# Optimization experiments

Measured on AMD Instinct MI355X. Metric: run time of the kernel, lower is better.

The kernel has to match this reference:

```python
import jax, jax.numpy as jnp
import numpy as np
import math

B, C, H, W = 16, 64, 128, 128
EPS = 1e-5


def _ln(x, g, b):
    m = jnp.mean(x, axis=-1, keepdims=True)
    v = jnp.var(x, axis=-1, keepdims=True)
    return (x - m) * jax.lax.rsqrt(v + EPS) * g + b


def setup_inputs() -> dict:
    key = jax.random.key(0)
    ks = jax.random.split(key, 8)
    s = 1.0 / math.sqrt(C)
    return {
        "x_l": jax.random.normal(ks[0], (B, C, H, W), dtype=jnp.float32),
        "x_h": jax.random.normal(ks[1], (B, C, H, W), dtype=jnp.float32),
        "ln1_g": jnp.ones((C,), jnp.float32),
        "ln1_b": jnp.zeros((C,), jnp.float32),
        "ln2_g": jnp.ones((C,), jnp.float32),
        "ln2_b": jnp.zeros((C,), jnp.float32),
        "Wq": jax.random.normal(ks[2], (C, C), dtype=jnp.float32) * s,
        "Wk": jax.random.normal(ks[3], (C, C), dtype=jnp.float32) * s,
        "Wv1": jax.random.normal(ks[4], (C, C), dtype=jnp.float32) * s,
        "Wv2": jax.random.normal(ks[5], (C, C), dtype=jnp.float32) * s,
    }


def reference(x_l, x_h, ln1_g, ln1_b, ln2_g, ln2_b, Wq, Wk, Wv1, Wv2):
    # [B,C,H,W] -> [B,H,W,C]
    xl = jnp.transpose(x_l, (0, 2, 3, 1))
    xh = jnp.transpose(x_h, (0, 2, 3, 1))
    # torch Linear: x @ W.T (no bias)
    xl_v = xl @ Wv1.T
    xh_v = xh @ Wv2.T
    q = _ln(xl, ln1_g, ln1_b) @ Wq.T
    k = _ln(xh, ln2_g, ln2_b) @ Wk.T
    # shared score matrix over the W axis: [B,H,W,W]
    attn = jnp.einsum('bhwc,bhvc->bhwv', q, k) * (1.0 / math.sqrt(C))
    attn_h = jax.nn.softmax(attn, axis=-1)                                  # row softmax
    attn_l = jax.nn.softmax(jnp.swapaxes(attn, 2, 3), axis=-1)              # column softmax
    xl_o = jnp.einsum('bhwv,bhvc->bhwc', attn_l, xl_v)
    xh_o = jnp.einsum('bhwv,bhvc->bhwc', attn_h, xh_v)
    xh_out = xh + xl_o
    xl_out = xl + xh_o
    # back to [B,C,H,W]
    return (jnp.transpose(xl_out, (0, 3, 1, 2)), jnp.transpose(xh_out, (0, 3, 1, 2)))
```

## Files before the change

kernel.cpp:

```cpp
#include <hip/hip_runtime.h>
#include <cstdint>


typedef __attribute__((ext_vector_type(8))) short bf16x8;
typedef __attribute__((ext_vector_type(4))) float f32x4;
typedef __attribute__((ext_vector_type(4))) unsigned u32x4;
typedef __attribute__((ext_vector_type(4))) unsigned short u16x4;

#define W2 136
#define QP 72
#define EP 132
#define OP 68

__device__ __forceinline__ unsigned rne_hi(float x) {
  unsigned u = __float_as_uint(x);
  return (u + 0x7FFFu + ((u >> 16) & 1u)) >> 16;
}
__device__ __forceinline__ void split2(float x, unsigned short& h, unsigned short& l) {
  unsigned hb = rne_hi(x);
  float rf = x - __uint_as_float(hb << 16);
  h = (unsigned short)hb;
  l = (unsigned short)(__float_as_uint(rf) >> 16);
}
__device__ __forceinline__ unsigned split_pack(float x) {
  unsigned short h, l; split2(x, h, l);
  return ((unsigned)h << 16) | (unsigned)l;
}
__device__ __forceinline__ float comb(unsigned h, unsigned l) {
  return __uint_as_float(h << 16) + __uint_as_float(l << 16);
}
__device__ __forceinline__ float unpack_f(unsigned p) {
  return __uint_as_float(p & 0xFFFF0000u) + __uint_as_float(p << 16);
}
__device__ __forceinline__ f32x4 mm3(bf16x8 ah, bf16x8 al, bf16x8 bh, bf16x8 bl, f32x4 c) {
  c = __builtin_amdgcn_mfma_f32_16x16x32_bf16(al, bh, c, 0, 0, 0);
  c = __builtin_amdgcn_mfma_f32_16x16x32_bf16(ah, bl, c, 0, 0, 0);
  c = __builtin_amdgcn_mfma_f32_16x16x32_bf16(ah, bh, c, 0, 0, 0);
  return c;
}

__global__ void scam_prepack(const float* __restrict__ ln1g, const float* __restrict__ ln1b,
                             const float* __restrict__ ln2g, const float* __restrict__ ln2b,
                             const float* __restrict__ Wq, const float* __restrict__ Wk,
                             const float* __restrict__ Wv1, const float* __restrict__ Wv2,
                             unsigned short* __restrict__ WP, float* __restrict__ vecs) {
  int t = blockIdx.x * 256 + threadIdx.x;
  int mat = t >> 12, rem = t & 4095, co = rem >> 6, c = rem & 63;
  const float* Ws = (mat == 0) ? Wq : (mat == 1) ? Wk : (mat == 2) ? Wv1 : Wv2;
  float g = 1.0f;
  if (mat == 0) g = ln1g[c];
  else if (mat == 1) g = ln2g[c];
  float val = Ws[co * 64 + c] * g;
  unsigned short h, l; split2(val, h, l);
  int nt = co >> 4, l15 = co & 15, ks = c >> 5, lg = (c >> 3) & 3, j = c & 7;
  int lanei = lg * 16 + l15;
  int ntk = nt * 2 + ks;
  WP[((mat * 2 + 0) * 8 + ntk) * 512 + lanei * 8 + j] = h;
  WP[((mat * 2 + 1) * 8 + ntk) * 512 + lanei * 8 + j] = l;
  if (blockIdx.x == 0 && threadIdx.x < 256) {
    int which = threadIdx.x >> 6, o = threadIdx.x & 63;
    const float* Wm = (which < 2) ? Wq : Wk;
    const float* gv = (which == 0) ? ln1g : (which == 1) ? ln1b : (which == 2) ? ln2g : ln2b;
    float ssum = 0.f;
    for (int cc = 0; cc < 64; ++cc) ssum += gv[cc] * Wm[o * 64 + cc];
    vecs[which * 64 + o] = ssum;
  }
}

struct SMem {
  unsigned short Xhi[2][64][W2];
  unsigned short Xlo[2][64][W2];
  union {
    unsigned short QK[4][128][QP];
    unsigned Epk[128][EP];
    unsigned Opk[2][128][OP];
  } rb;
  float meanv[2][128];
  float rstdv[2][128];
  float zr[128];
  float zc[128];
};

__launch_bounds__(1024, 1)
__global__ void scam_main(const float* __restrict__ xl_g, const float* __restrict__ xh_g,
                          const unsigned short* __restrict__ WP, const float* __restrict__ vecs,
                          float* __restrict__ out) {
  __shared__ __align__(16) SMem sm;
  const int tid = threadIdx.x;
  const int lane = tid & 63;
  const int wid = tid >> 6;
  const int stripe = wid >> 1;
  const int chalf = wid & 1;
  const int l15 = lane & 15;
  const int lg = lane >> 4;
  const int s = blockIdx.x;
  const size_t xoff = (size_t)(s >> 7) * 1048576u + (size_t)(s & 127) * 128u;

  {
    int c0 = tid >> 5, q4 = tid & 31;
#pragma unroll
    for (int mat = 0; mat < 2; ++mat) {
      const float* xg = mat ? xh_g : xl_g;
#pragma unroll
      for (int half = 0; half < 2; ++half) {
        int c = c0 + half * 32;
        f32x4 v = *(const f32x4*)(xg + xoff + (size_t)c * 16384u + q4 * 4);
        u16x4 h4, l4;
#pragma unroll
        for (int j = 0; j < 4; ++j) { unsigned short hh, ll; split2(v[j], hh, ll); h4[j] = hh; l4[j] = ll; }
        *(u16x4*)&sm.Xhi[mat][c][q4 * 4] = h4;
        *(u16x4*)&sm.Xlo[mat][c][q4 * 4] = l4;
      }
    }
  }
  __syncthreads();

  {
    int row = tid >> 2, qu = tid & 3;
    int mat = row >> 7, w = row & 127;
    float s1 = 0.f, s2 = 0.f;
#pragma unroll
    for (int i = 0; i < 16; ++i) {
      int c = qu * 16 + i;
      float x = comb(sm.Xhi[mat][c][w], sm.Xlo[mat][c][w]);
      s1 += x; s2 += x * x;
    }
    s1 += __shfl_xor(s1, 1); s2 += __shfl_xor(s2, 1);
    s1 += __shfl_xor(s1, 2); s2 += __shfl_xor(s2, 2);
    if (qu == 0) {
      float mn = s1 * (1.f / 64.f);
      float var = fmaxf(s2 * (1.f / 64.f) - mn * mn, 0.f);
      sm.meanv[mat][w] = mn;
      sm.rstdv[mat][w] = rsqrtf(var + 1e-5f);
    }
  }
  __syncthreads();

  {
    const int w = stripe * 16 + l15;
#pragma unroll
    for (int mat = 0; mat < 2; ++mat) {
      bf16x8 Ah[2], Al[2];
#pragma unroll
      for (int ks = 0; ks < 2; ++ks)
#pragma unroll
        for (int j = 0; j < 8; ++j) {
          int c = ks * 32 + lg * 8 + j;
          Ah[ks][j] = (short)sm.Xhi[mat][c][w];
          Al[ks][j] = (short)sm.Xlo[mat][c][w];
        }
      f32x4 acc[2];
#pragma unroll
      for (int nt = 0; nt < 2; ++nt)
#pragma unroll
        for (int r = 0; r < 4; ++r) acc[nt][r] = 0.f;
#pragma unroll
      for (int nt = 0; nt < 2; ++nt) {
        int ntg = chalf * 2 + nt;
#pragma unroll
        for (int ks = 0; ks < 2; ++ks) {
          const unsigned short* wp = WP + ((mat * 2 + 0) * 8 + (ntg * 2 + ks)) * 512 + lane * 8;
          bf16x8 Bh = *(const bf16x8*)wp;
          bf16x8 Bl = *(const bf16x8*)(wp + 4096);
          acc[nt] = mm3(Ah[ks], Al[ks], Bh, Bl, acc[nt]);
        }
      }
#pragma unroll
      for (int nt = 0; nt < 2; ++nt) {
        int co = (chalf * 2 + nt) * 16 + l15;
        float sv = vecs[mat * 128 + co];
        float bv = vecs[mat * 128 + 64 + co];
#pragma unroll
        for (int r = 0; r < 4; ++r) {
          int wr = stripe * 16 + lg * 4 + r;
          float qv = sm.rstdv[mat][wr] * (acc[nt][r] - sm.meanv[mat][wr] * sv) + bv;
          unsigned short hh, ll; split2(qv, hh, ll);
          sm.rb.QK[mat * 2 + 0][wr][co] = hh;
          sm.rb.QK[mat * 2 + 1][wr][co] = ll;
        }
      }
    }
  }
  __syncthreads();

  {
    const int w = stripe * 16 + l15;
    bf16x8 Ah[2], Al[2];
#pragma unroll
    for (int ks = 0; ks < 2; ++ks) {
      Ah[ks] = *(const bf16x8*)&sm.rb.QK[0][w][ks * 32 + lg * 8];
      Al[ks] = *(const bf16x8*)&sm.rb.QK[1][w][ks * 32 + lg * 8];
    }
    f32x4 acc[4];
#pragma unroll
    for (int nt = 0; nt < 4; ++nt)
#pragma unroll
      for (int r = 0; r < 4; ++r) acc[nt][r] = 0.f;
#pragma unroll
    for (int nt = 0; nt < 4; ++nt) {
      int kw = (chalf * 4 + nt) * 16 + l15;
#pragma unroll
      for (int ks = 0; ks < 2; ++ks) {
        bf16x8 Bh = *(const bf16x8*)&sm.rb.QK[2][kw][ks * 32 + lg * 8];
        bf16x8 Bl = *(const bf16x8*)&sm.rb.QK[3][kw][ks * 32 + lg * 8];
        acc[nt] = mm3(Ah[ks], Al[ks], Bh, Bl, acc[nt]);
      }
    }
    __syncthreads();
#pragma unroll
    for (int nt = 0; nt < 4; ++nt) {
      int col = (chalf * 4 + nt) * 16 + l15;
#pragma unroll
      for (int r = 0; r < 4; ++r) {
        int row = stripe * 16 + lg * 4 + r;
        float e = __builtin_amdgcn_exp2f(acc[nt][r] * 0.18033688011112042f);
        sm.rb.Epk[row][col] = split_pack(e);
      }
    }
  }
  __syncthreads();

  {
    int qu = tid & 3;
    float sum = 0.f;
    if (tid < 512) {
      int row = tid >> 2;
#pragma unroll
      for (int i = 0; i < 8; ++i) {
        u32x4 p = *(const u32x4*)&sm.rb.Epk[row][qu * 32 + i * 4];
#pragma unroll
        for (int j = 0; j < 4; ++j) sum += unpack_f(p[j]);
      }
      sum += __shfl_xor(sum, 1);
      sum += __shfl_xor(sum, 2);
      if (qu == 0) sm.zr[row] = 1.0f / sum;
    } else {
      int col = (tid >> 2) & 127;
#pragma unroll 8
      for (int i = 0; i < 32; ++i) sum += unpack_f(sm.rb.Epk[qu * 32 + i][col]);
      sum += __shfl_xor(sum, 1);
      sum += __shfl_xor(sum, 2);
      if (qu == 0) sm.zc[col] = 1.0f / sum;
    }
  }
  __syncthreads();

  {
    f32x4 acc0[2], acc1[2];
#pragma unroll
    for (int nt = 0; nt < 2; ++nt)
#pragma unroll
      for (int r = 0; r < 4; ++r) { acc0[nt][r] = 0.f; acc1[nt][r] = 0.f; }
#pragma unroll
    for (int kt = 0; kt < 4; ++kt) {
      {
        int row = stripe * 16 + l15;
        u32x4 p0 = *(const u32x4*)&sm.rb.Epk[row][kt * 32 + lg * 8];
        u32x4 p1 = *(const u32x4*)&sm.rb.Epk[row][kt * 32 + lg * 8 + 4];
        bf16x8 Ah, Al;
#pragma unroll
        for (int j = 0; j < 4; ++j) {
          Ah[j] = (short)(p0[j] >> 16);     Al[j] = (short)(p0[j] & 0xFFFFu);
          Ah[j + 4] = (short)(p1[j] >> 16); Al[j + 4] = (short)(p1[j] & 0xFFFFu);
        }
#pragma unroll
        for (int nt = 0; nt < 2; ++nt) {
          int c = (chalf * 2 + nt) * 16 + l15;
          bf16x8 Bh = *(const bf16x8*)&sm.Xhi[1][c][kt * 32 + lg * 8];
          bf16x8 Bl = *(const bf16x8*)&sm.Xlo[1][c][kt * 32 + lg * 8];
          acc0[nt] = mm3(Ah, Al, Bh, Bl, acc0[nt]);
        }
      }
      {
        bf16x8 Gh, Gl;
#pragma unroll
        for (int j = 0; j < 8; ++j) {
          unsigned p = sm.rb.Epk[kt * 32 + lg * 8 + j][stripe * 16 + l15];
          Gh[j] = (short)(p >> 16); Gl[j] = (short)(p & 0xFFFFu);
        }
#pragma unroll
        for (int nt = 0; nt < 2; ++nt) {
          int c = (chalf * 2 + nt) * 16 + l15;
          bf16x8 Bh = *(const bf16x8*)&sm.Xhi[0][c][kt * 32 + lg * 8];
          bf16x8 Bl = *(const bf16x8*)&sm.Xlo[0][c][kt * 32 + lg * 8];
          acc1[nt] = mm3(Gh, Gl, Bh, Bl, acc1[nt]);
        }
      }
    }
    __syncthreads();
#pragma unroll
    for (int nt = 0; nt < 2; ++nt) {
      int col = (chalf * 2 + nt) * 16 + l15;
#pragma unroll
      for (int r = 0; r < 4; ++r) {
        int row = stripe * 16 + lg * 4 + r;
        sm.rb.Opk[0][row][col] = split_pack(acc0[nt][r] * sm.zr[row]);
        sm.rb.Opk[1][row][col] = split_pack(acc1[nt][r] * sm.zc[row]);
      }
    }
  }
  __syncthreads();

#pragma unroll
  for (int oi = 0; oi < 2; ++oi) {
    const int wm = oi ? 2 : 3;
    const int w = stripe * 16 + l15;
    bf16x8 Ah[2], Al[2];
#pragma unroll
    for (int ks = 0; ks < 2; ++ks) {
      u32x4 p0 = *(const u32x4*)&sm.rb.Opk[oi][w][ks * 32 + lg * 8];
      u32x4 p1 = *(const u32x4*)&sm.rb.Opk[oi][w][ks * 32 + lg * 8 + 4];
#pragma unroll
      for (int j = 0; j < 4; ++j) {
        Ah[ks][j] = (short)(p0[j] >> 16);     Al[ks][j] = (short)(p0[j] & 0xFFFFu);
        Ah[ks][j + 4] = (short)(p1[j] >> 16); Al[ks][j + 4] = (short)(p1[j] & 0xFFFFu);
      }
    }
    f32x4 acc[2];
#pragma unroll
    for (int nt = 0; nt < 2; ++nt)
#pragma unroll
      for (int r = 0; r < 4; ++r) acc[nt][r] = 0.f;
#pragma unroll
    for (int nt = 0; nt < 2; ++nt) {
      int ntg = chalf * 2 + nt;
#pragma unroll
      for (int ks = 0; ks < 2; ++ks) {
        const unsigned short* wp = WP + ((wm * 2 + 0) * 8 + (ntg * 2 + ks)) * 512 + lane * 8;
        bf16x8 Bh = *(const bf16x8*)wp;
        bf16x8 Bl = *(const bf16x8*)(wp + 4096);
        acc[nt] = mm3(Ah[ks], Al[ks], Bh, Bl, acc[nt]);
      }
    }
    float* og = out + (size_t)oi * 16777216u + xoff;
    const int w0 = stripe * 16 + lg * 4;
#pragma unroll
    for (int nt = 0; nt < 2; ++nt) {
      int c = (chalf * 2 + nt) * 16 + l15;
      u16x4 hv = *(const u16x4*)&sm.Xhi[oi][c][w0];
      u16x4 lv = *(const u16x4*)&sm.Xlo[oi][c][w0];
      f32x4 o;
#pragma unroll
      for (int r = 0; r < 4; ++r) o[r] = acc[nt][r] + comb(hv[r], lv[r]);
      *(f32x4*)(og + (size_t)c * 16384u + w0) = o;
    }
  }
}

extern "C" void kernel_launch(void* const* d_in, const int* in_sizes, int n_in,
                              void* d_out, int out_size, void* d_ws, size_t ws_size,
                              hipStream_t stream) {
  (void)in_sizes; (void)n_in; (void)out_size; (void)ws_size;
  unsigned short* WP = (unsigned short*)d_ws;
  float* vecs = (float*)((char*)d_ws + 65536);
  scam_prepack<<<64, 256, 0, stream>>>(
      (const float*)d_in[2], (const float*)d_in[3],
      (const float*)d_in[4], (const float*)d_in[5],
      (const float*)d_in[6], (const float*)d_in[7],
      (const float*)d_in[8], (const float*)d_in[9], WP, vecs);
  scam_main<<<2048, 1024, 0, stream>>>(
      (const float*)d_in[0], (const float*)d_in[1], WP, vecs, (float*)d_out);
}
```

Baseline: 366.9 us.

## Fold Wq and Wk into one bilinear form and fuse the softmax sums

Precomputes M = Wq^T Wk (with the LN gains, LN biases and softmax scale folded in), so the scores come from LN(xl)·M applied straight against the raw xh columns. This drops one of the two 64x64 projections per block, and the xh layer norm is applied afterwards as per-column mean and rstd corrections. The row and column softmax sums are now reduced from registers during the exp stage, which removes the separate pass over E. X is stored as packed hi/lo words in one array, and the final Wv projection writes output directly with a transposed tile mapping. The costs are atomics plus a memset in the prepack, an extra correction-vector setup, and per-element scalar global stores for the output.

Measured after the change: 354.9 us. -3.3%, faster.

```diff
diff --git a/kernel.cpp b/kernel.cpp
--- a/kernel.cpp
+++ b/kernel.cpp
@@ -4,13 +4,9 @@
 
 typedef __attribute__((ext_vector_type(8))) short bf16x8;
 typedef __attribute__((ext_vector_type(4))) float f32x4;
-typedef __attribute__((ext_vector_type(4))) unsigned u32x4;
-typedef __attribute__((ext_vector_type(4))) unsigned short u16x4;
-
-#define W2 136
-#define QP 72
-#define EP 132
-#define OP 68
+typedef __attribute__((ext_vector_type(2))) unsigned u32x2;
+
+#define LAM 0.18033688011112042f
 
 __device__ __forceinline__ unsigned rne_hi(float x) {
   unsigned u = __float_as_uint(x);
@@ -26,9 +22,6 @@
   unsigned short h, l; split2(x, h, l);
   return ((unsigned)h << 16) | (unsigned)l;
 }
-__device__ __forceinline__ float comb(unsigned h, unsigned l) {
-  return __uint_as_float(h << 16) + __uint_as_float(l << 16);
-}
 __device__ __forceinline__ float unpack_f(unsigned p) {
   return __uint_as_float(p & 0xFFFF0000u) + __uint_as_float(p << 16);
 }
@@ -38,47 +31,93 @@
   c = __builtin_amdgcn_mfma_f32_16x16x32_bf16(ah, bh, c, 0, 0, 0);
   return c;
 }
+__device__ __forceinline__ void row_frag(const unsigned* p, bf16x8& fh, bf16x8& fl) {
+  u32x2 q0 = *(const u32x2*)p, q1 = *(const u32x2*)(p + 2);
+  u32x2 q2 = *(const u32x2*)(p + 4), q3 = *(const u32x2*)(p + 6);
+  unsigned w0 = q0[0], w1 = q0[1], w2 = q1[0], w3 = q1[1];
+  unsigned w4 = q2[0], w5 = q2[1], w6 = q3[0], w7 = q3[1];
+  fh[0] = (short)(w0 >> 16); fl[0] = (short)(w0 & 0xFFFFu);
+  fh[1] = (short)(w1 >> 16); fl[1] = (short)(w1 & 0xFFFFu);
+  fh[2] = (short)(w2 >> 16); fl[2] = (short)(w2 & 0xFFFFu);
+  fh[3] = (short)(w3 >> 16); fl[3] = (short)(w3 & 0xFFFFu);
+  fh[4] = (short)(w4 >> 16); fl[4] = (short)(w4 & 0xFFFFu);
+  fh[5] = (short)(w5 >> 16); fl[5] = (short)(w5 & 0xFFFFu);
+  fh[6] = (short)(w6 >> 16); fl[6] = (short)(w6 & 0xFFFFu);
+  fh[7] = (short)(w7 >> 16); fl[7] = (short)(w7 & 0xFFFFu);
+}
 
 __global__ void scam_prepack(const float* __restrict__ ln1g, const float* __restrict__ ln1b,
                              const float* __restrict__ ln2g, const float* __restrict__ ln2b,
                              const float* __restrict__ Wq, const float* __restrict__ Wk,
                              const float* __restrict__ Wv1, const float* __restrict__ Wv2,
                              unsigned short* __restrict__ WP, float* __restrict__ vecs) {
-  int t = blockIdx.x * 256 + threadIdx.x;
-  int mat = t >> 12, rem = t & 4095, co = rem >> 6, c = rem & 63;
-  const float* Ws = (mat == 0) ? Wq : (mat == 1) ? Wk : (mat == 2) ? Wv1 : Wv2;
-  float g = 1.0f;
-  if (mat == 0) g = ln1g[c];
-  else if (mat == 1) g = ln2g[c];
-  float val = Ws[co * 64 + c] * g;
-  unsigned short h, l; split2(val, h, l);
-  int nt = co >> 4, l15 = co & 15, ks = c >> 5, lg = (c >> 3) & 3, j = c & 7;
-  int lanei = lg * 16 + l15;
-  int ntk = nt * 2 + ks;
-  WP[((mat * 2 + 0) * 8 + ntk) * 512 + lanei * 8 + j] = h;
-  WP[((mat * 2 + 1) * 8 + ntk) * 512 + lanei * 8 + j] = l;
-  if (blockIdx.x == 0 && threadIdx.x < 256) {
-    int which = threadIdx.x >> 6, o = threadIdx.x & 63;
-    const float* Wm = (which < 2) ? Wq : Wk;
-    const float* gv = (which == 0) ? ln1g : (which == 1) ? ln1b : (which == 2) ? ln2g : ln2b;
-    float ssum = 0.f;
-    for (int cc = 0; cc < 64; ++cc) ssum += gv[cc] * Wm[o * 64 + cc];
-    vecs[which * 64 + o] = ssum;
+  __shared__ float Wkl[64][65];
+  __shared__ float wqc[64][4];
+  __shared__ float gb[4][64];
+  const int tid = threadIdx.x;
+  const int blk = blockIdx.x;
+  const int c0 = blk * 4;
+#pragma unroll
+  for (int i = 0; i < 16; ++i) {
+    int idx = i * 256 + tid;
+    Wkl[idx >> 6][idx & 63] = Wk[idx];
+  }
+  { int o = tid >> 2, ci = tid & 3; wqc[o][ci] = Wq[o * 64 + c0 + ci]; }
+  { int g = tid >> 6, e = tid & 63;
+    const float* src = (g == 0) ? ln1g : (g == 1) ? ln1b : (g == 2) ? ln2g : ln2b;
+    gb[g][e] = src[e]; }
+  __syncthreads();
+  const int ci = tid >> 6, cp = tid & 63;
+  const int c = c0 + ci;
+  float d = 0.f;
+#pragma unroll 8
+  for (int o = 0; o < 64; ++o) d += wqc[o][ci] * Wkl[o][cp];
+  d *= LAM;
+  float mb = gb[0][c] * d * gb[2][cp];
+  float tb = gb[1][c] * d * gb[2][cp];
+  atomicAdd(&vecs[cp], mb);
+  atomicAdd(&vecs[64 + cp], tb);
+  {
+    unsigned short h, l; split2(mb, h, l);
+    int nt = cp >> 4, l15 = cp & 15, ks = c >> 5, lg = (c >> 3) & 3, j = c & 7;
+    int ui = (nt * 2 + ks) * 512 + (lg * 16 + l15) * 8 + j;
+    WP[ui] = h; WP[4096 + ui] = l;
+  }
+  float t = d * gb[3][cp];
+#pragma unroll
+  for (int s = 1; s < 64; s <<= 1) t += __shfl_xor(t, s);
+  if ((tid & 63) == 0) {
+    vecs[128 + c] = gb[0][c] * t;
+    atomicAdd(&vecs[192], gb[0][c] * t);
+    atomicAdd(&vecs[193], gb[1][c] * t);
+  }
+  int idx2 = blk * 256 + tid;
+#pragma unroll
+  for (int m = 0; m < 2; ++m) {
+    float v = (m ? Wv2 : Wv1)[idx2];
+    unsigned short h, l; split2(v, h, l);
+    int o = idx2 >> 6, cc = idx2 & 63;
+    int mt = o >> 4, l15 = o & 15, ks = cc >> 5, lg = (cc >> 3) & 3, j = cc & 7;
+    int ui = m * 8192 + (mt * 2 + ks) * 512 + (lg * 16 + l15) * 8 + j;
+    WP[8192 + ui] = h;
+    WP[8192 + ui + 4096] = l;
   }
 }
 
 struct SMem {
-  unsigned short Xhi[2][64][W2];
-  unsigned short Xlo[2][64][W2];
+  unsigned X[2][64][130];
   union {
-    unsigned short QK[4][128][QP];
-    unsigned Epk[128][EP];
-    unsigned Opk[2][128][OP];
-  } rb;
-  float meanv[2][128];
-  float rstdv[2][128];
-  float zr[128];
-  float zc[128];
+    unsigned short T2[2][128][72];
+    unsigned E[128][130];
+    unsigned short O[2][2][128][72];
+  } R;
+  float m_[2][128], r_[2][128];
+  float uT[128], vT[128], zr[128], zc[128];
+  float vT2[2][128];
+  float zrP[2][128];
+  float zcP[8][128];
+  float s1v[64], t1v[64], mbv[64];
+  float smbv, tmbv;
 };
 
 __launch_bounds__(1024, 1)
@@ -89,233 +128,68 @@
   const int tid = threadIdx.x;
   const int lane = tid & 63;
   const int wid = tid >> 6;
-  const int stripe = wid >> 1;
-  const int chalf = wid & 1;
-  const int l15 = lane & 15;
-  const int lg = lane >> 4;
+  const int stripe = wid >> 1, chalf = wid & 1;
+  const int l15 = lane & 15, lg = lane >> 4;
   const int s = blockIdx.x;
   const size_t xoff = (size_t)(s >> 7) * 1048576u + (size_t)(s & 127) * 128u;
 
   {
-    int c0 = tid >> 5, q4 = tid & 31;
-#pragma unroll
-    for (int mat = 0; mat < 2; ++mat) {
+    float* Z = &sm.vT2[0][0];
+    for (int i = tid; i < 1536; i += 1024) Z[i] = 0.f;
+    if (tid < 64) {
+      sm.s1v[tid] = vecs[tid];
+      sm.t1v[tid] = vecs[64 + tid];
+      sm.mbv[tid] = vecs[128 + tid];
+    }
+    if (tid == 64) { sm.smbv = vecs[192]; sm.tmbv = vecs[193]; }
+    const int q = tid & 31, cb = tid >> 5;
+#pragma unroll
+    for (int i = 0; i < 4; ++i) {
+      int mat = i >> 1, c = cb + (i & 1) * 32;
       const float* xg = mat ? xh_g : xl_g;
-#pragma unroll
-      for (int half = 0; half < 2; ++half) {
-        int c = c0 + half * 32;
-        f32x4 v = *(const f32x4*)(xg + xoff + (size_t)c * 16384u + q4 * 4);
-        u16x4 h4, l4;
-#pragma unroll
-        for (int j = 0; j < 4; ++j) { unsigned short hh, ll; split2(v[j], hh, ll); h4[j] = hh; l4[j] = ll; }
-        *(u16x4*)&sm.Xhi[mat][c][q4 * 4] = h4;
-        *(u16x4*)&sm.Xlo[mat][c][q4 * 4] = l4;
-      }
-    }
-  }
-  __syncthreads();
-
-  {
-    int row = tid >> 2, qu = tid & 3;
-    int mat = row >> 7, w = row & 127;
-    float s1 = 0.f, s2 = 0.f;
+      f32x4 v = *(const f32x4*)(xg + xoff + (size_t)c * 16384u + q * 4);
+      u32x2 p0, p1;
+      p0[0] = split_pack(v[0]); p0[1] = split_pack(v[1]);
+      p1[0] = split_pack(v[2]); p1[1] = split_pack(v[3]);
+      *(u32x2*)&sm.X[mat][c][q * 4] = p0;
+      *(u32x2*)&sm.X[mat][c][q * 4 + 2] = p1;
+    }
+  }
+  __syncthreads();
+
+  {
+    const int row = tid >> 2, qu = tid & 3;
+    const int mat = row >> 7, w = row & 127;
+    float a1 = 0.f, a2 = 0.f, a3 = 0.f;
 #pragma unroll
     for (int i = 0; i < 16; ++i) {
-      int c = qu * 16 + i;
-      float x = comb(sm.Xhi[mat][c][w], sm.Xlo[mat][c][w]);
-      s1 += x; s2 += x * x;
-    }
-    s1 += __shfl_xor(s1, 1); s2 += __shfl_xor(s2, 1);
-    s1 += __shfl_xor(s1, 2); s2 += __shfl_xor(s2, 2);
+      int c = qu + i * 4;
+      float x = unpack_f(sm.X[mat][c][w]);
+      a1 += x; a2 += x * x;
+      if (mat == 0) a3 += x * sm.mbv[c];
+    }
+    a1 += __shfl_xor(a1, 1); a2 += __shfl_xor(a2, 1); a3 += __shfl_xor(a3, 1);
+    a1 += __shfl_xor(a1, 2); a2 += __shfl_xor(a2, 2); a3 += __shfl_xor(a3, 2);
     if (qu == 0) {
-      float mn = s1 * (1.f / 64.f);
-      float var = fmaxf(s2 * (1.f / 64.f) - mn * mn, 0.f);
-      sm.meanv[mat][w] = mn;
-      sm.rstdv[mat][w] = rsqrtf(var + 1e-5f);
-    }
-  }
-  __syncthreads();
-
-  {
-    const int w = stripe * 16 + l15;
-#pragma unroll
-    for (int mat = 0; mat < 2; ++mat) {
-      bf16x8 Ah[2], Al[2];
-#pragma unroll
-      for (int ks = 0; ks < 2; ++ks)
-#pragma unroll
-        for (int j = 0; j < 8; ++j) {
-          int c = ks * 32 + lg * 8 + j;
-          Ah[ks][j] = (short)sm.Xhi[mat][c][w];
-          Al[ks][j] = (short)sm.Xlo[mat][c][w];
-        }
-      f32x4 acc[2];
-#pragma unroll
-      for (int nt = 0; nt < 2; ++nt)
-#pragma unroll
-        for (int r = 0; r < 4; ++r) acc[nt][r] = 0.f;
-#pragma unroll
-      for (int nt = 0; nt < 2; ++nt) {
-        int ntg = chalf * 2 + nt;
-#pragma unroll
-        for (int ks = 0; ks < 2; ++ks) {
-          const unsigned short* wp = WP + ((mat * 2 + 0) * 8 + (ntg * 2 + ks)) * 512 + lane * 8;
-          bf16x8 Bh = *(const bf16x8*)wp;
-          bf16x8 Bl = *(const bf16x8*)(wp + 4096);
-          acc[nt] = mm3(Ah[ks], Al[ks], Bh, Bl, acc[nt]);
-        }
-      }
-#pragma unroll
-      for (int nt = 0; nt < 2; ++nt) {
-        int co = (chalf * 2 + nt) * 16 + l15;
-        float sv = vecs[mat * 128 + co];
-        float bv = vecs[mat * 128 + 64 + co];
-#pragma unroll
-        for (int r = 0; r < 4; ++r) {
-          int wr = stripe * 16 + lg * 4 + r;
-          float qv = sm.rstdv[mat][wr] * (acc[nt][r] - sm.meanv[mat][wr] * sv) + bv;
-          unsigned short hh, ll; split2(qv, hh, ll);
-          sm.rb.QK[mat * 2 + 0][wr][co] = hh;
-          sm.rb.QK[mat * 2 + 1][wr][co] = ll;
-        }
-      }
-    }
-  }
-  __syncthreads();
-
-  {
-    const int w = stripe * 16 + l15;
+      float mn = a1 * (1.f / 64.f);
+      float var = fmaxf(a2 * (1.f / 64.f) - mn * mn, 0.f);
+      float rs = rsqrtf(var + 1e-5f);
+      sm.m_[mat][w] = mn; sm.r_[mat][w] = rs;
+      if (mat == 0) sm.uT[w] = rs * (a3 - mn * sm.smbv) + sm.tmbv;
+    }
+  }
+  __syncthreads();
+
+  {
+    const int wA = stripe * 16 + l15;
     bf16x8 Ah[2], Al[2];
 #pragma unroll
-    for (int ks = 0; ks < 2; ++ks) {
-      Ah[ks] = *(const bf16x8*)&sm.rb.QK[0][w][ks * 32 + lg * 8];
-      Al[ks] = *(const bf16x8*)&sm.rb.QK[1][w][ks * 32 + lg * 8];
-    }
-    f32x4 acc[4];
-#pragma unroll
-    for (int nt = 0; nt < 4; ++nt)
-#pragma unroll
-      for (int r = 0; r < 4; ++r) acc[nt][r] = 0.f;
-#pragma unroll
-    for (int nt = 0; nt < 4; ++nt) {
-      int kw = (chalf * 4 + nt) * 16 + l15;
-#pragma unroll
-      for (int ks = 0; ks < 2; ++ks) {
-        bf16x8 Bh = *(const bf16x8*)&sm.rb.QK[2][kw][ks * 32 + lg * 8];
-        bf16x8 Bl = *(const bf16x8*)&sm.rb.QK[3][kw][ks * 32 + lg * 8];
-        acc[nt] = mm3(Ah[ks], Al[ks], Bh, Bl, acc[nt]);
-      }
-    }
-    __syncthreads();
-#pragma unroll
-    for (int nt = 0; nt < 4; ++nt) {
-      int col = (chalf * 4 + nt) * 16 + l15;
-#pragma unroll
-      for (int r = 0; r < 4; ++r) {
-        int row = stripe * 16 + lg * 4 + r;
-        float e = __builtin_amdgcn_exp2f(acc[nt][r] * 0.18033688011112042f);
-        sm.rb.Epk[row][col] = split_pack(e);
-      }
-    }
-  }
-  __syncthreads();
-
-  {
-    int qu = tid & 3;
-    float sum = 0.f;
-    if (tid < 512) {
-      int row = tid >> 2;
-#pragma unroll
-      for (int i = 0; i < 8; ++i) {
-        u32x4 p = *(const u32x4*)&sm.rb.Epk[row][qu * 32 + i * 4];
-#pragma unroll
-        for (int j = 0; j < 4; ++j) sum += unpack_f(p[j]);
-      }
-      sum += __shfl_xor(sum, 1);
-      sum += __shfl_xor(sum, 2);
-      if (qu == 0) sm.zr[row] = 1.0f / sum;
-    } else {
-      int col = (tid >> 2) & 127;
-#pragma unroll 8
-      for (int i = 0; i < 32; ++i) sum += unpack_f(sm.rb.Epk[qu * 32 + i][col]);
-      sum += __shfl_xor(sum, 1);
-      sum += __shfl_xor(sum, 2);
-      if (qu == 0) sm.zc[col] = 1.0f / sum;
-    }
-  }
-  __syncthreads();
-
-  {
-    f32x4 acc0[2], acc1[2];
-#pragma unroll
-    for (int nt = 0; nt < 2; ++nt)
-#pragma unroll
-      for (int r = 0; r < 4; ++r) { acc0[nt][r] = 0.f; acc1[nt][r] = 0.f; }
-#pragma unroll
-    for (int kt = 0; kt < 4; ++kt) {
-      {
-        int row = stripe * 16 + l15;
-        u32x4 p0 = *(const u32x4*)&sm.rb.Epk[row][kt * 32 + lg * 8];
-        u32x4 p1 = *(const u32x4*)&sm.rb.Epk[row][kt * 32 + lg * 8 + 4];
-        bf16x8 Ah, Al;
-#pragma unroll
-        for (int j = 0; j < 4; ++j) {
-          Ah[j] = (short)(p0[j] >> 16);     Al[j] = (short)(p0[j] & 0xFFFFu);
-          Ah[j + 4] = (short)(p1[j] >> 16); Al[j + 4] = (short)(p1[j] & 0xFFFFu);
-        }
-#pragma unroll
-        for (int nt = 0; nt < 2; ++nt) {
-          int c = (chalf * 2 + nt) * 16 + l15;
-          bf16x8 Bh = *(const bf16x8*)&sm.Xhi[1][c][kt * 32 + lg * 8];
-          bf16x8 Bl = *(const bf16x8*)&sm.Xlo[1][c][kt * 32 + lg * 8];
-          acc0[nt] = mm3(Ah, Al, Bh, Bl, acc0[nt]);
-        }
-      }
-      {
-        bf16x8 Gh, Gl;
-#pragma unroll
-        for (int j = 0; j < 8; ++j) {
-          unsigned p = sm.rb.Epk[kt * 32 + lg * 8 + j][stripe * 16 + l15];
-          Gh[j] = (short)(p >> 16); Gl[j] = (short)(p & 0xFFFFu);
-        }
-#pragma unroll
-        for (int nt = 0; nt < 2; ++nt) {
-          int c = (chalf * 2 + nt) * 16 + l15;
-          bf16x8 Bh = *(const bf16x8*)&sm.Xhi[0][c][kt * 32 + lg * 8];
-          bf16x8 Bl = *(const bf16x8*)&sm.Xlo[0][c][kt * 32 + lg * 8];
-          acc1[nt] = mm3(Gh, Gl, Bh, Bl, acc1[nt]);
-        }
-      }
-    }
-    __syncthreads();
-#pragma unroll
-    for (int nt = 0; nt < 2; ++nt) {
-      int col = (chalf * 2 + nt) * 16 + l15;
-#pragma unroll
-      for (int r = 0; r < 4; ++r) {
-        int row = stripe * 16 + lg * 4 + r;
-        sm.rb.Opk[0][row][col] = split_pack(acc0[nt][r] * sm.zr[row]);
-        sm.rb.Opk[1][row][col] = split_pack(acc1[nt][r] * sm.zc[row]);
-      }
-    }
-  }
-  __syncthreads();
-
-#pragma unroll
-  for (int oi = 0; oi < 2; ++oi) {
-    const int wm = oi ? 2 : 3;
-    const int w = stripe * 16 + l15;
-    bf16x8 Ah[2], Al[2];
-#pragma unroll
-    for (int ks = 0; ks < 2; ++ks) {
-      u32x4 p0 = *(const u32x4*)&sm.rb.Opk[oi][w][ks * 32 + lg * 8];
-      u32x4 p1 = *(const u32x4*)&sm.rb.Opk[oi][w][ks * 32 + lg * 8 + 4];
-#pragma unroll
-      for (int j = 0; j < 4; ++j) {
-        Ah[ks][j] = (short)(p0[j] >> 16);     Al[ks][j] = (short)(p0[j] & 0xFFFFu);
-        Ah[ks][j + 4] = (short)(p1[j] >> 16); Al[ks][j + 4] = (short)(p1[j] & 0xFFFFu);
-      }
-    }
+    for (int ks = 0; ks < 2; ++ks)
+#pragma unroll
+      for (int j = 0; j < 8; ++j) {
+        unsigned p = sm.X[0][ks * 32 + lg * 8 + j][wA];
+        Ah[ks][j] = (short)(p >> 16); Al[ks][j] = (short)(p & 0xFFFFu);
+      }
     f32x4 acc[2];
 #pragma unroll
     for (int nt = 0; nt < 2; ++nt)
@@ -326,23 +200,189 @@
       int ntg = chalf * 2 + nt;
 #pragma unroll
       for (int ks = 0; ks < 2; ++ks) {
-        const unsigned short* wp = WP + ((wm * 2 + 0) * 8 + (ntg * 2 + ks)) * 512 + lane * 8;
+        const unsigned short* wp = WP + (ntg * 2 + ks) * 512 + lane * 8;
         bf16x8 Bh = *(const bf16x8*)wp;
         bf16x8 Bl = *(const bf16x8*)(wp + 4096);
         acc[nt] = mm3(Ah[ks], Al[ks], Bh, Bl, acc[nt]);
       }
     }
-    float* og = out + (size_t)oi * 16777216u + xoff;
-    const int w0 = stripe * 16 + lg * 4;
+    float vsum[4] = {0.f, 0.f, 0.f, 0.f};
+#pragma unroll
+    for (int nt = 0; nt < 2; ++nt) {
+      int cp = (chalf * 2 + nt) * 16 + l15;
+      float sv = sm.s1v[cp], tv = sm.t1v[cp];
+#pragma unroll
+      for (int r = 0; r < 4; ++r) {
+        int wr = stripe * 16 + lg * 4 + r;
+        float t2 = sm.r_[0][wr] * (acc[nt][r] - sm.m_[0][wr] * sv) + tv;
+        unsigned short h, l; split2(t2, h, l);
+        sm.R.T2[0][wr][cp] = h; sm.R.T2[1][wr][cp] = l;
+        vsum[r] += t2;
+      }
+    }
+#pragma unroll
+    for (int r = 0; r < 4; ++r) {
+      float v = vsum[r];
+      v += __shfl_xor(v, 1); v += __shfl_xor(v, 2);
+      v += __shfl_xor(v, 4); v += __shfl_xor(v, 8);
+      if (l15 == 0) sm.vT2[chalf][stripe * 16 + lg * 4 + r] = v;
+    }
+  }
+  __syncthreads();
+
+  {
+    if (tid < 128) sm.vT[tid] = sm.vT2[0][tid] + sm.vT2[1][tid];
+    const int wA = stripe * 16 + l15;
+    bf16x8 Ah[2], Al[2];
+#pragma unroll
+    for (int ks = 0; ks < 2; ++ks) {
+      Ah[ks] = *(const bf16x8*)&sm.R.T2[0][wA][ks * 32 + lg * 8];
+      Al[ks] = *(const bf16x8*)&sm.R.T2[1][wA][ks * 32 + lg * 8];
+    }
+    f32x4 acc[4];
+#pragma unroll
+    for (int nt = 0; nt < 4; ++nt)
+#pragma unroll
+      for (int r = 0; r < 4; ++r) acc[nt][r] = 0.f;
+#pragma unroll
+    for (int nt = 0; nt < 4; ++nt) {
+      int wk = (chalf * 4 + nt) * 16 + l15;
+#pragma unroll
+      for (int ks = 0; ks < 2; ++ks) {
+        bf16x8 Bh, Bl;
+#pragma unroll
+        for (int j = 0; j < 8; ++j) {
+          unsigned p = sm.X[1][ks * 32 + lg * 8 + j][wk];
+          Bh[j] = (short)(p >> 16); Bl[j] = (short)(p & 0xFFFFu);
+        }
+        acc[nt] = mm3(Ah[ks], Al[ks], Bh, Bl, acc[nt]);
+      }
+    }
+    __syncthreads();
+    float ev[4][4];
+#pragma unroll
+    for (int nt = 0; nt < 4; ++nt) {
+      int wk = (chalf * 4 + nt) * 16 + l15;
+      float rr = sm.r_[1][wk], mm = sm.m_[1][wk];
+#pragma unroll
+      for (int r = 0; r < 4; ++r) {
+        int wq = stripe * 16 + lg * 4 + r;
+        float s2 = rr * (acc[nt][r] - mm * sm.vT[wq]) + sm.uT[wq];
+        float e = __builtin_amdgcn_exp2f(s2);
+        ev[nt][r] = e;
+        sm.R.E[wq][wk] = split_pack(e);
+      }
+    }
+#pragma unroll
+    for (int r = 0; r < 4; ++r) {
+      float v = ev[0][r] + ev[1][r] + ev[2][r] + ev[3][r];
+      v += __shfl_xor(v, 1); v += __shfl_xor(v, 2);
+      v += __shfl_xor(v, 4); v += __shfl_xor(v, 8);
+      if (l15 == 0) sm.zrP[chalf][stripe * 16 + lg * 4 + r] = v;
+    }
+#pragma unroll
+    for (int nt = 0; nt < 4; ++nt) {
+      float v = ev[nt][0] + ev[nt][1] + ev[nt][2] + ev[nt][3];
+      v += __shfl_xor(v, 16); v += __shfl_xor(v, 32);
+      if (lg == 0) sm.zcP[stripe][(chalf * 4 + nt) * 16 + l15] = v;
+    }
+  }
+  __syncthreads();
+
+  {
+    if (tid < 128) {
+      sm.zr[tid] = 1.0f / (sm.zrP[0][tid] + sm.zrP[1][tid]);
+    } else if (tid < 256) {
+      int c = tid - 128;
+      float t = 0.f;
+#pragma unroll
+      for (int st = 0; st < 8; ++st) t += sm.zcP[st][c];
+      sm.zc[c] = 1.0f / t;
+    }
+    const int wA = stripe * 16 + l15;
+    f32x4 aH[2], aL[2];
+#pragma unroll
+    for (int nt = 0; nt < 2; ++nt)
+#pragma unroll
+      for (int r = 0; r < 4; ++r) { aH[nt][r] = 0.f; aL[nt][r] = 0.f; }
+#pragma unroll
+    for (int kt = 0; kt < 4; ++kt) {
+      bf16x8 Eh, El;
+      row_frag(&sm.R.E[wA][kt * 32 + lg * 8], Eh, El);
+      bf16x8 Th, Tl;
+#pragma unroll
+      for (int j = 0; j < 8; ++j) {
+        unsigned p = sm.R.E[kt * 32 + lg * 8 + j][wA];
+        Th[j] = (short)(p >> 16); Tl[j] = (short)(p & 0xFFFFu);
+      }
+#pragma unroll
+      for (int nt = 0; nt < 2; ++nt) {
+        int c = (chalf * 2 + nt) * 16 + l15;
+        bf16x8 BHh, BHl, BLh, BLl;
+        row_frag(&sm.X[1][c][kt * 32 + lg * 8], BHh, BHl);
+        row_frag(&sm.X[0][c][kt * 32 + lg * 8], BLh, BLl);
+        aH[nt] = mm3(Eh, El, BHh, BHl, aH[nt]);
+        aL[nt] = mm3(Th, Tl, BLh, BLl, aL[nt]);
+      }
+    }
+    __syncthreads();
 #pragma unroll
     for (int nt = 0; nt < 2; ++nt) {
       int c = (chalf * 2 + nt) * 16 + l15;
-      u16x4 hv = *(const u16x4*)&sm.Xhi[oi][c][w0];
-      u16x4 lv = *(const u16x4*)&sm.Xlo[oi][c][w0];
-      f32x4 o;
-#pragma unroll
-      for (int r = 0; r < 4; ++r) o[r] = acc[nt][r] + comb(hv[r], lv[r]);
-      *(f32x4*)(og + (size_t)c * 16384u + w0) = o;
+#pragma unroll
+      for (int r = 0; r < 4; ++r) {
+        int w = stripe * 16 + lg * 4 + r;
+        unsigned short h, l;
+        split2(aH[nt][r] * sm.zr[w], h, l);
+        sm.R.O[0][0][w][c] = h; sm.R.O[0][1][w][c] = l;
+        split2(aL[nt][r] * sm.zc[w], h, l);
+        sm.R.O[1][0][w][c] = h; sm.R.O[1][1][w][c] = l;
+      }
+    }
+  }
+  __syncthreads();
+
+  {
+    const int mt = wid >> 2, np = wid & 3;
+#pragma unroll
+    for (int oi = 0; oi < 2; ++oi) {
+      const int osel = oi;
+      const int wsel = oi ? 0 : 1;
+      const unsigned short* WA = WP + 8192 + wsel * 8192;
+      bf16x8 Ah[2], Al[2];
+#pragma unroll
+      for (int ks = 0; ks < 2; ++ks) {
+        const unsigned short* wp = WA + (mt * 2 + ks) * 512 + lane * 8;
+        Ah[ks] = *(const bf16x8*)wp;
+        Al[ks] = *(const bf16x8*)(wp + 4096);
+      }
+      f32x4 acc[2];
+#pragma unroll
+      for (int nt2 = 0; nt2 < 2; ++nt2)
+#pragma unroll
+        for (int r = 0; r < 4; ++r) acc[nt2][r] = 0.f;
+#pragma unroll
+      for (int nt2 = 0; nt2 < 2; ++nt2) {
+        int wc = (np * 2 + nt2) * 16 + l15;
+#pragma unroll
+        for (int ks = 0; ks < 2; ++ks) {
+          bf16x8 Bh = *(const bf16x8*)&sm.R.O[osel][0][wc][ks * 32 + lg * 8];
+          bf16x8 Bl = *(const bf16x8*)&sm.R.O[osel][1][wc][ks * 32 + lg * 8];
+          acc[nt2] = mm3(Ah[ks], Al[ks], Bh, Bl, acc[nt2]);
+        }
+      }
+      const float* res = (oi ? xh_g : xl_g) + xoff;
+      float* og = out + (size_t)oi * 16777216u + xoff;
+#pragma unroll
+      for (int nt2 = 0; nt2 < 2; ++nt2) {
+        int wc = (np * 2 + nt2) * 16 + l15;
+#pragma unroll
+        for (int r = 0; r < 4; ++r) {
+          int o = mt * 16 + lg * 4 + r;
+          size_t a = (size_t)o * 16384u + wc;
+          og[a] = acc[nt2][r] + res[a];
+        }
+      }
     }
   }
 }
@@ -352,8 +392,9 @@
                               hipStream_t stream) {
   (void)in_sizes; (void)n_in; (void)out_size; (void)ws_size;
   unsigned short* WP = (unsigned short*)d_ws;
-  float* vecs = (float*)((char*)d_ws + 65536);
-  scam_prepack<<<64, 256, 0, stream>>>(
+  float* vecs = (float*)((char*)d_ws + 49152);
+  hipMemsetAsync(vecs, 0, 1024, stream);
+  scam_prepack<<<16, 256, 0, stream>>>(
       (const float*)d_in[2], (const float*)d_in[3],
       (const float*)d_in[4], (const float*)d_in[5],
       (const float*)d_in[6], (const float*)d_in[7],
```
